# Performance work log

Measured on AMD Instinct MI355X. Metric: run time of the kernel, lower is better.

The kernel has to match this reference:

```python
import jax, jax.numpy as jnp
import numpy as np

B, C, H, W = 2, 192, 128, 128
NUM_HEADS = 6
AMP = 1
NUM_OFFSETS = 9


def bilinear_sample(img, grid):
    # img: (C, H, W); grid: (Hn, Wn, 2) in [-1,1], align_corners=True, zeros padding
    Hh, Ww = img.shape[1], img.shape[2]
    x = (grid[..., 0] + 1.0) * 0.5 * (Ww - 1)
    y = (grid[..., 1] + 1.0) * 0.5 * (Hh - 1)
    x0 = jnp.floor(x)
    y0 = jnp.floor(y)
    x1 = x0 + 1.0
    y1 = y0 + 1.0
    wx1 = x - x0
    wy1 = y - y0

    def gather(yi, xi):
        valid = ((xi >= 0) & (xi <= Ww - 1) & (yi >= 0) & (yi <= Hh - 1)).astype(img.dtype)
        xc = jnp.clip(xi, 0, Ww - 1).astype(jnp.int32)
        yc = jnp.clip(yi, 0, Hh - 1).astype(jnp.int32)
        return img[:, yc, xc] * valid  # (C, Hn, Wn)

    return (gather(y0, x0) * ((1 - wy1) * (1 - wx1))
            + gather(y0, x1) * ((1 - wy1) * wx1)
            + gather(y1, x0) * (wy1 * (1 - wx1))
            + gather(y1, x1) * (wy1 * wx1))


def setup_inputs() -> dict:
    key = jax.random.key(0)
    ks = jax.random.split(key, 8)
    s = 0.02
    Ch = C // NUM_HEADS
    return {
        "x_q": jax.random.normal(ks[0], (B, C, H, W), jnp.float32),
        "x_kv": jax.random.normal(ks[1], (B, C, H, W), jnp.float32),
        "w_q": jax.random.normal(ks[2], (C, C), jnp.float32) * s,
        "w_kv": jax.random.normal(ks[3], (2 * C, C), jnp.float32) * s,
        "w_off1": jax.random.normal(ks[4], (C, 2 * C, 3, 3), jnp.float32) * s,
        "b_off1": jnp.zeros((C,), jnp.float32),
        "w_off2": jax.random.normal(ks[5], (2 * NUM_OFFSETS, C), jnp.float32) * s,
        "b_off2": jnp.zeros((2 * NUM_OFFSETS,), jnp.float32),
        "w_proj": jax.random.normal(ks[6], (C, C), jnp.float32) * s,
        "b_proj": jnp.zeros((C,), jnp.float32),
    }


def reference(x_q, x_kv, w_q, w_kv, w_off1, b_off1, w_off2, b_off2, w_proj, b_proj):
    Ch = C // NUM_HEADS
    scale = Ch ** (-0.5)

    # 1x1 conv projections as channel matmuls
    q = jnp.einsum('oc,bchw->bohw', w_q, x_q) * scale
    kv = jnp.einsum('oc,bchw->bohw', w_kv, x_kv)
    k, v = kv[:, :C], kv[:, C:]  # kv.reshape(B,2,Ch,nh,H,W) -> first C channels are k

    # offset predictor: 3x3 conv -> relu -> 1x1 conv
    off_in = jnp.concatenate([x_q, x_kv], axis=1)
    h1 = jax.lax.conv_general_dilated(off_in, w_off1, (1, 1), 'SAME',
                                      dimension_numbers=('NCHW', 'OIHW', 'NCHW'))
    h1 = jax.nn.relu(h1 + b_off1[None, :, None, None])
    off = jnp.einsum('oc,bchw->bohw', w_off2, h1) + b_off2[None, :, None, None]
    off = off.reshape(B, NUM_OFFSETS, 2, H, W).transpose(0, 1, 3, 4, 2)  # (B,9,H,W,2)
    gx = off[..., 0] / (W - 1) * 2.0 - 1.0
    gy = off[..., 1] / (H - 1) * 2.0 - 1.0
    grid = jnp.stack([gx, gy], axis=-1)  # (B,9,H,W,2)

    # deformable gather: sample full-channel k/v at each of 9 per-pixel offset grids
    sample = jax.vmap(jax.vmap(bilinear_sample, in_axes=(None, 0)), in_axes=(0, 0))
    k_s = sample(k, grid).reshape(B, NUM_OFFSETS, Ch, NUM_HEADS, H, W)
    v_s = sample(v, grid).reshape(B, NUM_OFFSETS, Ch, NUM_HEADS, H, W)

    q = q.reshape(B, Ch, NUM_HEADS, H, W)

    pad = [(0, 0), (0, 0), (0, 0), (0, 0), (AMP, AMP), (AMP, AMP)]
    k_p = jnp.pad(k_s, pad)
    v_p = jnp.pad(v_s, pad)

    win = 2 * AMP + 1
    logits = []
    for i in range(win):
        for j in range(win):
            idx = i * win + j
            kp = k_p[:, idx, :, :, i:i + H, j:j + W]  # (B,Ch,nh,H,W)
            logits.append(jnp.einsum('bchxy,bchxy->bhxy', q, kp))
    attn = jax.nn.softmax(jnp.stack(logits, axis=1), axis=1)  # (B,9,nh,H,W)

    out = jnp.zeros((B, Ch, NUM_HEADS, H, W), x_q.dtype)
    for i in range(win):
        for j in range(win):
            idx = i * win + j
            vp = v_p[:, idx, :, :, i:i + H, j:j + W]
            out = out + attn[:, idx, None] * vp

    out = out.reshape(B, C, H, W)  # channel layout = (Ch, nh), matching torch reshape
    return jnp.einsum('oc,bchw->bohw', w_proj, out) + b_proj[None, :, None, None]
```

## Files before the change

kernel.cpp:

```cpp
#include <hip/hip_runtime.h>
#include <math.h>

#define HW 16384
#define NB 2
#define NC 192

typedef __attribute__((ext_vector_type(8))) short bh8;
typedef __attribute__((ext_vector_type(4))) float f32x4;

__device__ inline ushort f2bf(float f) {
  union { float f; unsigned int u; } x; x.f = f;
  unsigned int r = x.u + 0x7fffu + ((x.u >> 16) & 1u);
  return (ushort)(r >> 16);
}
__device__ inline float bf2f(ushort u) {
  union { unsigned int i; float f; } x; x.i = ((unsigned int)u) << 16;
  return x.f;
}
__device__ inline void gl16(const ushort* g, char* l) {
  __builtin_amdgcn_global_load_lds(
      (const __attribute__((address_space(1))) unsigned int*)g,
      (__attribute__((address_space(3))) unsigned int*)l, 16, 0, 0);
}

__global__ void k_wpack(const float* __restrict__ w1, ushort* __restrict__ wpack) {
  int i = blockIdx.x * 256 + threadIdx.x;
  int s = i / 6144;
  int rem = i - s * 6144;
  int o = rem >> 5, kk = rem & 31;
  int dy = s / 36, t2 = s - dy * 36;
  int icc = t2 / 3, dxi = t2 - icc * 3;
  int ic = icc * 32 + kk;
  wpack[i] = f2bf(w1[(size_t)o * 3456 + (size_t)ic * 9 + dy * 3 + dxi]);
}

__global__ void k_wgpack(const float* __restrict__ wq, const float* __restrict__ wkv,
                         const float* __restrict__ wp, float scale,
                         ushort* __restrict__ wg) {
  int i = blockIdx.x * 256 + threadIdx.x;
  int r = i / NC, c = i - r * NC;
  float v;
  if (r < 192) {
    int orow = (r & 31) * 6 + (r >> 5);
    v = wq[(size_t)orow * NC + c] * scale;
  } else if (r < 576) {
    int rp = r - 192;
    int t = rp >= 192 ? 1 : 0;
    int cc = rp - t * 192;
    int orow = t * 192 + (cc & 31) * 6 + (cc >> 5);
    v = wkv[(size_t)orow * NC + c];
  } else {
    int rp = r - 576;
    v = wp[(size_t)rp * NC + ((c & 31) * 6 + (c >> 5))];
  }
  wg[i] = f2bf(v);
}

__global__ void k_zero(uint4* __restrict__ p) {
  p[(size_t)blockIdx.x * 256 + threadIdx.x] = make_uint4(0u, 0u, 0u, 0u);
}

__global__ __launch_bounds__(256) void k_xpack(const float* __restrict__ xq,
                                               const float* __restrict__ xkv,
                                               ushort* __restrict__ xpp) {
  __shared__ float t[NC][65];
  const int tid = threadIdx.x;
  const size_t r0 = (size_t)blockIdx.x * 64;
  const int b = (int)(r0 >> 14);
  const int px0 = (int)(r0 & 16383);
  const int y = px0 >> 7, x0 = px0 & 127;
  const float* src = (blockIdx.y == 0 ? xq : xkv) + (size_t)b * NC * HW + px0;
#pragma unroll
  for (int it = 0; it < 12; ++it) {
    int i = it * 256 + tid;
    int c = i >> 4, q4 = i & 15;
    float4 v = *(const float4*)(src + (size_t)c * HW + q4 * 4);
    t[c][q4 * 4 + 0] = v.x; t[c][q4 * 4 + 1] = v.y;
    t[c][q4 * 4 + 2] = v.z; t[c][q4 * 4 + 3] = v.w;
  }
  __syncthreads();
  ushort* dst = xpp + ((size_t)(b * 130 + y + 1) * 132 + x0 + 1) * 384 +
                blockIdx.y * 192;
#pragma unroll
  for (int it = 0; it < 6; ++it) {
    int i = it * 256 + tid;
    int px = i / 24, ch = i - px * 24;
    ushort4 u0, u1;
    u0.x = f2bf(t[ch * 8 + 0][px]); u0.y = f2bf(t[ch * 8 + 1][px]);
    u0.z = f2bf(t[ch * 8 + 2][px]); u0.w = f2bf(t[ch * 8 + 3][px]);
    u1.x = f2bf(t[ch * 8 + 4][px]); u1.y = f2bf(t[ch * 8 + 5][px]);
    u1.z = f2bf(t[ch * 8 + 6][px]); u1.w = f2bf(t[ch * 8 + 7][px]);
    *(ushort4*)&dst[(size_t)px * 384 + ch * 8] = u0;
    *(ushort4*)&dst[(size_t)px * 384 + ch * 8 + 4] = u1;
  }
}

__device__ inline void stage64(ushort* lds, const ushort* src, int rowStride,
                               int tid) {
#pragma unroll
  for (int it = 0; it < 6; ++it) {
    int i = it * 256 + tid;
    int row = i / 24, c = i - row * 24;
    int pos = (c & 24) | ((c & 7) ^ (row & 7));
    uint4 v = *(const uint4*)(src + (size_t)row * rowStride + c * 8);
    *(uint4*)&lds[row * NC + pos * 8] = v;
  }
}
__device__ inline bh8 frag64(const ushort* lds, int row, int c) {
  int pos = (c & 24) | ((c & 7) ^ (row & 7));
  return *(const bh8*)&lds[row * NC + pos * 8];
}

__global__ __launch_bounds__(256) void k_gemm_mfma(
    const ushort* __restrict__ xpp, int cOff, const ushort* __restrict__ wg,
    ushort* __restrict__ outA, ushort* __restrict__ outB) {
  __shared__ __attribute__((aligned(16))) ushort xs[64 * NC];
  __shared__ __attribute__((aligned(16))) ushort ws2[64 * NC];
  const int tid = threadIdx.x;
  const size_t p0 = (size_t)blockIdx.x * 64;
  const int bb = (int)(p0 >> 14);
  const int yy = (int)((p0 >> 7) & 127);
  const int xx0 = (int)(p0 & 127);
  const int o0 = blockIdx.y * 64;
  const ushort* src = xpp + ((size_t)(bb * 130 + yy + 1) * 132 + xx0 + 1) * 384 + cOff;
  stage64(xs, src, 384, tid);
  stage64(ws2, wg + (size_t)o0 * NC, NC, tid);
  __syncthreads();
  const int lid = tid & 15, g = (tid >> 4) & 3, wv = tid >> 6;
  const int wo = (wv & 1) * 32, wp = (wv >> 1) * 32;
  f32x4 acc[2][2];
#pragma unroll
  for (int m = 0; m < 2; ++m)
#pragma unroll
    for (int n = 0; n < 2; ++n) acc[m][n] = (f32x4){0.f, 0.f, 0.f, 0.f};
#pragma unroll
  for (int k = 0; k < 6; ++k) {
    bh8 a0 = frag64(ws2, wo + lid, k * 4 + g);
    bh8 a1 = frag64(ws2, wo + 16 + lid, k * 4 + g);
    bh8 b0 = frag64(xs, wp + lid, k * 4 + g);
    bh8 b1 = frag64(xs, wp + 16 + lid, k * 4 + g);
    acc[0][0] = __builtin_amdgcn_mfma_f32_16x16x32_bf16(a0, b0, acc[0][0], 0, 0, 0);
    acc[0][1] = __builtin_amdgcn_mfma_f32_16x16x32_bf16(a0, b1, acc[0][1], 0, 0, 0);
    acc[1][0] = __builtin_amdgcn_mfma_f32_16x16x32_bf16(a1, b0, acc[1][0], 0, 0, 0);
    acc[1][1] = __builtin_amdgcn_mfma_f32_16x16x32_bf16(a1, b1, acc[1][1], 0, 0, 0);
  }
  const int t = o0 >= 192 ? 1 : 0;
  ushort* dst = t ? outB : outA;
  const int od = o0 - t * 192;
#pragma unroll
  for (int m = 0; m < 2; ++m)
#pragma unroll
    for (int n = 0; n < 2; ++n) {
      int orow = od + wo + m * 16 + g * 4;
      size_t px = p0 + wp + n * 16 + lid;
      ushort4 u;
      u.x = f2bf(acc[m][n][0]); u.y = f2bf(acc[m][n][1]);
      u.z = f2bf(acc[m][n][2]); u.w = f2bf(acc[m][n][3]);
      *(ushort4*)&dst[px * NC + orow] = u;
    }
}

__global__ __launch_bounds__(256) void k_proj_mfma(
    const ushort* __restrict__ pre, const ushort* __restrict__ wg,
    const float* __restrict__ bp, float* __restrict__ out) {
  __shared__ __attribute__((aligned(16))) ushort xs[64 * NC];
  __shared__ __attribute__((aligned(16))) ushort ws2[64 * NC];
  const int tid = threadIdx.x;
  const size_t p0 = (size_t)blockIdx.x * 64;
  const int o0 = blockIdx.y * 64;
  stage64(xs, pre + p0 * NC, NC, tid);
  stage64(ws2, wg + (size_t)o0 * NC, NC, tid);
  __syncthreads();
  const int lid = tid & 15, g = (tid >> 4) & 3, wv = tid >> 6;
  const int wo = (wv & 1) * 32, wp = (wv >> 1) * 32;
  f32x4 acc[2][2];
#pragma unroll
  for (int m = 0; m < 2; ++m)
#pragma unroll
    for (int n = 0; n < 2; ++n) acc[m][n] = (f32x4){0.f, 0.f, 0.f, 0.f};
#pragma unroll
  for (int k = 0; k < 6; ++k) {
    bh8 a0 = frag64(ws2, wo + lid, k * 4 + g);
    bh8 a1 = frag64(ws2, wo + 16 + lid, k * 4 + g);
    bh8 b0 = frag64(xs, wp + lid, k * 4 + g);
    bh8 b1 = frag64(xs, wp + 16 + lid, k * 4 + g);
    acc[0][0] = __builtin_amdgcn_mfma_f32_16x16x32_bf16(a0, b0, acc[0][0], 0, 0, 0);
    acc[0][1] = __builtin_amdgcn_mfma_f32_16x16x32_bf16(a0, b1, acc[0][1], 0, 0, 0);
    acc[1][0] = __builtin_amdgcn_mfma_f32_16x16x32_bf16(a1, b0, acc[1][0], 0, 0, 0);
    acc[1][1] = __builtin_amdgcn_mfma_f32_16x16x32_bf16(a1, b1, acc[1][1], 0, 0, 0);
  }
#pragma unroll
  for (int m = 0; m < 2; ++m)
#pragma unroll
    for (int n = 0; n < 2; ++n) {
      int oc = o0 + wo + m * 16 + g * 4;
      size_t pxf = p0 + wp + n * 16 + lid;
      int b = (int)(pxf >> 14);
      int px = (int)(pxf & 16383);
#pragma unroll
      for (int j = 0; j < 4; ++j)
        out[((size_t)b * NC + oc + j) * HW + px] = acc[m][n][j] + bp[oc + j];
    }
}

#define CP0 0
#define CP1 8448
#define CW0 16896
#define CW1 35328
__global__ __launch_bounds__(256, 3) void k_conv_mfma(
    const ushort* __restrict__ xpp, const ushort* __restrict__ wpack,
    const float* __restrict__ b1, ushort* __restrict__ h1) {
  __shared__ __attribute__((aligned(16))) char smem[53760];
  const int tid = threadIdx.x;
  const int bi = blockIdx.x;
  const int b = bi >> 8;
  const int y = (bi >> 1) & 127;
  const int oh = bi & 1;
  const int lid = tid & 15;
  const int g = (tid >> 4) & 3;
  const int wv = tid >> 6;
  const int lane = tid & 63;
  const int og = wv & 1;
  const int pg = wv >> 1;
  f32x4 acc[3][4];
#pragma unroll
  for (int m = 0; m < 3; ++m)
#pragma unroll
    for (int n = 0; n < 4; ++n) acc[m][n] = (f32x4){0.f, 0.f, 0.f, 0.f};

  auto stageP = [&](int icc, int dy, int buf) {
    const size_t rowbase = (size_t)(b * 130 + y + dy) * 132 * 384 + icc * 32;
    char* dst0 = smem + (buf ? CP1 : CP0);
    for (int grp = wv; grp < 9; grp += 4) {
      int i = grp * 64 + lane;
      if (i < 528) {
        int slot = i >> 2, ch = i & 3;
        gl16(xpp + rowbase + (size_t)slot * 384 + ((ch ^ ((slot >> 1) & 3)) << 3),
             dst0 + grp * 1024);
      }
    }
  };
  auto stageW = [&](int icc, int dy, int buf) {
    const ushort* wsrc = wpack + (size_t)((dy * 12 + icc) * 3) * 6144 + oh * 96 * 32;
    char* dst0 = smem + (buf ? CW1 : CW0);
    for (int grp = wv; grp < 18; grp += 4) {
      int i = grp * 64 + lane;
      int dxi = i / 384;
      int rem = i - dxi * 384;
      int o = rem >> 2, q = rem & 3;
      gl16(wsrc + (size_t)dxi * 6144 + o * 32 + ((q ^ ((o >> 1) & 3)) << 3),
           dst0 + grp * 1024);
    }
  };

  stageP(0, 0, 0);
  stageW(0, 0, 0);
  __syncthreads();
  int cur = 0;
  for (int s = 0; s < 36; ++s) {
    if (s < 35) {
      const int ns = s + 1;
      const int nicc = ns / 3, ndy = ns - nicc * 3;
      stageP(nicc, ndy, cur ^ 1);
      stageW(nicc, ndy, cur ^ 1);
    }
    const char* Pb = smem + (cur ? CP1 : CP0);
    const char* Wb = smem + (cur ? CW1 : CW0);
#pragma unroll
    for (int dxi = 0; dxi < 3; ++dxi) {
      bh8 af[3];
#pragma unroll
      for (int m = 0; m < 3; ++m) {
        int o = og * 48 + m * 16 + lid;
        af[m] = *(const bh8*)(Wb + ((dxi * 96 + o) << 6) +
                              ((g ^ ((o >> 1) & 3)) << 4));
      }
#pragma unroll
      for (int n = 0; n < 4; ++n) {
        int slot = pg * 64 + n * 16 + lid + dxi;
        bh8 bf = *(const bh8*)(Pb + (slot << 6) + ((g ^ ((slot >> 1) & 3)) << 4));
#pragma unroll
        for (int m = 0; m < 3; ++m)
          acc[m][n] = __builtin_amdgcn_mfma_f32_16x16x32_bf16(
              af[m], bf, acc[m][n], 0, 0, 0);
      }
    }
    __syncthreads();
    cur ^= 1;
  }

  const size_t pxbase = (size_t)(b << 14) + y * 128 + pg * 64;
#pragma unroll
  for (int m = 0; m < 3; ++m) {
    const int ob = oh * 96 + og * 48 + m * 16 + g * 4;
    float4 bv = *(const float4*)(b1 + ob);
#pragma unroll
    for (int n = 0; n < 4; ++n) {
      size_t px = pxbase + n * 16 + lid;
      h1[(size_t)(ob + 0) * (NB * HW) + px] = f2bf(fmaxf(acc[m][n][0] + bv.x, 0.f));
      h1[(size_t)(ob + 1) * (NB * HW) + px] = f2bf(fmaxf(acc[m][n][1] + bv.y, 0.f));
      h1[(size_t)(ob + 2) * (NB * HW) + px] = f2bf(fmaxf(acc[m][n][2] + bv.z, 0.f));
      h1[(size_t)(ob + 3) * (NB * HW) + px] = f2bf(fmaxf(acc[m][n][3] + bv.w, 0.f));
    }
  }
}

__global__ __launch_bounds__(256) void k_offhead(
    const ushort* __restrict__ h1, const float* __restrict__ w2,
    const float* __restrict__ b2, float* __restrict__ off) {
  __shared__ float w2l[18 * NC];
  const int tid = threadIdx.x;
  for (int i = tid; i < 18 * NC; i += 256) w2l[i] = w2[i];
  __syncthreads();
  const int px = tid & 127;
  const int jh = tid >> 7;
  const size_t p = (size_t)blockIdx.x * 128 + px;
  float acc[9];
#pragma unroll
  for (int jj = 0; jj < 9; ++jj) acc[jj] = b2[jh * 9 + jj];
  for (int c = 0; c < NC; ++c) {
    float v = bf2f(h1[(size_t)c * (NB * HW) + p]);
#pragma unroll
    for (int jj = 0; jj < 9; ++jj) acc[jj] += w2l[(jh * 9 + jj) * NC + c] * v;
  }
#pragma unroll
  for (int jj = 0; jj < 9; ++jj) off[p * 18 + jh * 9 + jj] = acc[jj];
}

__global__ __launch_bounds__(256) void k_attn(
    const ushort* __restrict__ q, const ushort* __restrict__ k,
    const ushort* __restrict__ v, const float* __restrict__ off,
    ushort* __restrict__ pre) {
  __shared__ float slog[4][6][9];
  __shared__ float sattn[4][6][9];
  const int wv = threadIdx.x >> 6;
  const int lane = threadIdx.x & 63;
  const size_t p = (size_t)blockIdx.x * 4 + wv;
  const int b = (int)(p >> 14);
  const int pp = (int)(p & 16383);
  const int y = pp >> 7, x = pp & 127;
  const ushort* qrow = q + p * NC;
  float qv0 = bf2f(qrow[lane]), qv1 = bf2f(qrow[lane + 64]), qv2 = bf2f(qrow[lane + 128]);
  float vsr[9][3];
#pragma unroll
  for (int idx = 0; idx < 9; ++idx) {
    const int di = idx / 3 - 1, dj = idx % 3 - 1;
    const int yy = y + di, xx = x + dj;
    const bool inb = (yy >= 0) && (yy < 128) && (xx >= 0) && (xx < 128);
    float ks0 = 0.f, ks1 = 0.f, ks2 = 0.f;
    float v0 = 0.f, v1 = 0.f, v2 = 0.f;
    if (inb) {
      const size_t sp = (size_t)b * HW + yy * 128 + xx;
      const float sx = off[sp * 18 + idx * 2 + 0];
      const float sy = off[sp * 18 + idx * 2 + 1];
      const float fx0 = floorf(sx), fy0 = floorf(sy);
      const float wx = sx - fx0, wy = sy - fy0;
#pragma unroll
      for (int cyx = 0; cyx < 4; ++cyx) {
        const int cy = cyx >> 1, cx = cyx & 1;
        const float xi = fx0 + cx, yi = fy0 + cy;
        const float wgt = (cx ? wx : 1.f - wx) * (cy ? wy : 1.f - wy);
        const bool okc = (xi >= 0.f) && (xi <= 127.f) && (yi >= 0.f) && (yi <= 127.f);
        if (okc) {
          const int xc = (int)xi, yc = (int)yi;
          const size_t cb = ((size_t)b * HW + yc * 128 + xc) * NC + lane;
          ks0 += wgt * bf2f(k[cb]);       v0 += wgt * bf2f(v[cb]);
          ks1 += wgt * bf2f(k[cb + 64]);  v1 += wgt * bf2f(v[cb + 64]);
          ks2 += wgt * bf2f(k[cb + 128]); v2 += wgt * bf2f(v[cb + 128]);
        }
      }
    }
    vsr[idx][0] = v0; vsr[idx][1] = v1; vsr[idx][2] = v2;
    float p0 = qv0 * ks0, p1 = qv1 * ks1, p2 = qv2 * ks2;
#pragma unroll
    for (int m = 16; m >= 1; m >>= 1) {
      p0 += __shfl_xor(p0, m);
      p1 += __shfl_xor(p1, m);
      p2 += __shfl_xor(p2, m);
    }
    if ((lane & 31) == 0) {
      const int hb = lane >> 5;
      slog[wv][hb + 0][idx] = p0;
      slog[wv][hb + 2][idx] = p1;
      slog[wv][hb + 4][idx] = p2;
    }
  }
  __syncthreads();
  if (lane < 6) {
    float mx = -1e30f;
#pragma unroll
    for (int i = 0; i < 9; ++i) mx = fmaxf(mx, slog[wv][lane][i]);
    float e[9];
    float s = 0.f;
#pragma unroll
    for (int i = 0; i < 9; ++i) { e[i] = expf(slog[wv][lane][i] - mx); s += e[i]; }
    const float inv = 1.f / s;
#pragma unroll
    for (int i = 0; i < 9; ++i) sattn[wv][lane][i] = e[i] * inv;
  }
  __syncthreads();
  float o0 = 0.f, o1 = 0.f, o2 = 0.f;
  const int hb = lane >> 5;
#pragma unroll
  for (int idx = 0; idx < 9; ++idx) {
    o0 += sattn[wv][hb + 0][idx] * vsr[idx][0];
    o1 += sattn[wv][hb + 2][idx] * vsr[idx][1];
    o2 += sattn[wv][hb + 4][idx] * vsr[idx][2];
  }
  ushort* prow = pre + p * NC;
  prow[lane] = f2bf(o0);
  prow[lane + 64] = f2bf(o1);
  prow[lane + 128] = f2bf(o2);
}

extern "C" void kernel_launch(void* const* d_in, const int* in_sizes, int n_in,
                              void* d_out, int out_size, void* d_ws, size_t ws_size,
                              hipStream_t stream) {
  const float* x_q    = (const float*)d_in[0];
  const float* x_kv   = (const float*)d_in[1];
  const float* w_q    = (const float*)d_in[2];
  const float* w_kv   = (const float*)d_in[3];
  const float* w_off1 = (const float*)d_in[4];
  const float* b_off1 = (const float*)d_in[5];
  const float* w_off2 = (const float*)d_in[6];
  const float* b_off2 = (const float*)d_in[7];
  const float* w_proj = (const float*)d_in[8];
  const float* b_proj = (const float*)d_in[9];
  float* out = (float*)d_out;

  char* W = (char*)d_ws;
  const size_t SB = (size_t)NB * HW * NC * 2;
  ushort* qb   = (ushort*)W;
  ushort* kb   = (ushort*)(W + SB);
  ushort* vb   = (ushort*)(W + 2 * SB);
  ushort* preb = (ushort*)(W + 3 * SB);
  ushort* h1b  = preb;
  ushort* wg   = (ushort*)(W + 4 * SB);
  ushort* xpp  = (ushort*)(W + 4 * SB + 294912);
  float*  offb = (float*)xpp;
  ushort* wpk  = (ushort*)d_out;

  const float scale = 0.17677669529663687f;
  dim3 blk(256);
  k_wpack<<<dim3(2592), blk, 0, stream>>>(w_off1, wpk);
  k_wgpack<<<dim3(576), blk, 0, stream>>>(w_q, w_kv, w_proj, scale, wg);
  k_zero<<<dim3(6435), blk, 0, stream>>>((uint4*)xpp);
  k_xpack<<<dim3(512, 2), blk, 0, stream>>>(x_q, x_kv, xpp);
  k_gemm_mfma<<<dim3(512, 3), blk, 0, stream>>>(xpp, 0, wg, qb, qb);
  k_gemm_mfma<<<dim3(512, 6), blk, 0, stream>>>(xpp, 192, wg + 192 * NC, kb, vb);
  k_conv_mfma<<<dim3(512), blk, 0, stream>>>(xpp, wpk, b_off1, h1b);
  k_offhead<<<dim3(NB * 128), blk, 0, stream>>>(h1b, w_off2, b_off2, offb);
  k_attn<<<dim3(8192), blk, 0, stream>>>(qb, kb, vb, offb, preb);
  k_proj_mfma<<<dim3(512, 3), blk, 0, stream>>>(preb, wg + 576 * NC, b_proj, out);
}
```

Baseline: 202.8 us.

## Vectorize deformable attention gathers and keep the softmax in registers

Each pixel's work is remapped so 48 lanes each own 4 contiguous bf16 channels. The q, k and v corner gathers become 8-byte vector loads, and the per-head dot products are reduced with three shuffles inside each 8-lane group. The shared-memory logits and attention buffers and both __syncthreads are removed, and the corner gathers use clamped indices with mask weights instead of branches. The intent is fewer, wider memory transactions and less synchronization. In exchange, 16 lanes per wave sit idle and the code uses fast exp and reciprocal intrinsics, which may change precision slightly.

```diff
diff --git a/kernel.cpp b/kernel.cpp
--- a/kernel.cpp
+++ b/kernel.cpp
@@ -16,6 +16,9 @@
 __device__ inline float bf2f(ushort u) {
   union { unsigned int i; float f; } x; x.i = ((unsigned int)u) << 16;
   return x.f;
+}
+__device__ inline float asf(unsigned int u) {
+  union { unsigned int i; float f; } x; x.i = u; return x.f;
 }
 __device__ inline void gl16(const ushort* g, char* l) {
   __builtin_amdgcn_global_load_lds(
@@ -331,86 +334,96 @@
     const ushort* __restrict__ q, const ushort* __restrict__ k,
     const ushort* __restrict__ v, const float* __restrict__ off,
     ushort* __restrict__ pre) {
-  __shared__ float slog[4][6][9];
-  __shared__ float sattn[4][6][9];
   const int wv = threadIdx.x >> 6;
   const int lane = threadIdx.x & 63;
+  if (lane >= 48) return;
   const size_t p = (size_t)blockIdx.x * 4 + wv;
   const int b = (int)(p >> 14);
   const int pp = (int)(p & 16383);
   const int y = pp >> 7, x = pp & 127;
-  const ushort* qrow = q + p * NC;
-  float qv0 = bf2f(qrow[lane]), qv1 = bf2f(qrow[lane + 64]), qv2 = bf2f(qrow[lane + 128]);
-  float vsr[9][3];
+
+  uint2 qu = *(const uint2*)(q + p * NC + 4 * lane);
+  const float q0 = asf(qu.x << 16), q1 = asf(qu.x & 0xffff0000u);
+  const float q2 = asf(qu.y << 16), q3 = asf(qu.y & 0xffff0000u);
+  const size_t cbase = (size_t)b * HW * NC + 4 * lane;
+  const size_t obase = (size_t)b * HW;
+
+  float pl[9];
+  float vsr[9][4];
 #pragma unroll
   for (int idx = 0; idx < 9; ++idx) {
-    const int di = idx / 3 - 1, dj = idx % 3 - 1;
-    const int yy = y + di, xx = x + dj;
+    const int yy = y + idx / 3 - 1, xx = x + idx % 3 - 1;
     const bool inb = (yy >= 0) && (yy < 128) && (xx >= 0) && (xx < 128);
-    float ks0 = 0.f, ks1 = 0.f, ks2 = 0.f;
-    float v0 = 0.f, v1 = 0.f, v2 = 0.f;
+    float sx = 0.f, sy = 0.f;
     if (inb) {
-      const size_t sp = (size_t)b * HW + yy * 128 + xx;
-      const float sx = off[sp * 18 + idx * 2 + 0];
-      const float sy = off[sp * 18 + idx * 2 + 1];
-      const float fx0 = floorf(sx), fy0 = floorf(sy);
-      const float wx = sx - fx0, wy = sy - fy0;
-#pragma unroll
-      for (int cyx = 0; cyx < 4; ++cyx) {
-        const int cy = cyx >> 1, cx = cyx & 1;
-        const float xi = fx0 + cx, yi = fy0 + cy;
-        const float wgt = (cx ? wx : 1.f - wx) * (cy ? wy : 1.f - wy);
-        const bool okc = (xi >= 0.f) && (xi <= 127.f) && (yi >= 0.f) && (yi <= 127.f);
-        if (okc) {
-          const int xc = (int)xi, yc = (int)yi;
-          const size_t cb = ((size_t)b * HW + yc * 128 + xc) * NC + lane;
-          ks0 += wgt * bf2f(k[cb]);       v0 += wgt * bf2f(v[cb]);
-          ks1 += wgt * bf2f(k[cb + 64]);  v1 += wgt * bf2f(v[cb + 64]);
-          ks2 += wgt * bf2f(k[cb + 128]); v2 += wgt * bf2f(v[cb + 128]);
-        }
-      }
-    }
-    vsr[idx][0] = v0; vsr[idx][1] = v1; vsr[idx][2] = v2;
-    float p0 = qv0 * ks0, p1 = qv1 * ks1, p2 = qv2 * ks2;
-#pragma unroll
-    for (int m = 16; m >= 1; m >>= 1) {
-      p0 += __shfl_xor(p0, m);
-      p1 += __shfl_xor(p1, m);
-      p2 += __shfl_xor(p2, m);
-    }
-    if ((lane & 31) == 0) {
-      const int hb = lane >> 5;
-      slog[wv][hb + 0][idx] = p0;
-      slog[wv][hb + 2][idx] = p1;
-      slog[wv][hb + 4][idx] = p2;
-    }
-  }
-  __syncthreads();
-  if (lane < 6) {
-    float mx = -1e30f;
-#pragma unroll
-    for (int i = 0; i < 9; ++i) mx = fmaxf(mx, slog[wv][lane][i]);
-    float e[9];
-    float s = 0.f;
-#pragma unroll
-    for (int i = 0; i < 9; ++i) { e[i] = expf(slog[wv][lane][i] - mx); s += e[i]; }
-    const float inv = 1.f / s;
-#pragma unroll
-    for (int i = 0; i < 9; ++i) sattn[wv][lane][i] = e[i] * inv;
-  }
-  __syncthreads();
-  float o0 = 0.f, o1 = 0.f, o2 = 0.f;
-  const int hb = lane >> 5;
-#pragma unroll
-  for (int idx = 0; idx < 9; ++idx) {
-    o0 += sattn[wv][hb + 0][idx] * vsr[idx][0];
-    o1 += sattn[wv][hb + 2][idx] * vsr[idx][1];
-    o2 += sattn[wv][hb + 4][idx] * vsr[idx][2];
-  }
-  ushort* prow = pre + p * NC;
-  prow[lane] = f2bf(o0);
-  prow[lane + 64] = f2bf(o1);
-  prow[lane + 128] = f2bf(o2);
+      const size_t sp = obase + yy * 128 + xx;
+      sx = off[sp * 18 + idx * 2 + 0];
+      sy = off[sp * 18 + idx * 2 + 1];
+    }
+    const float fx0 = floorf(sx), fy0 = floorf(sy);
+    const float wx1 = sx - fx0, wy1 = sy - fy0;
+    const float wx0 = 1.f - wx1, wy0 = 1.f - wy1;
+    const float inbf = inb ? 1.f : 0.f;
+    const float mx0 = (fx0 >= 0.f && fx0 <= 127.f) ? inbf : 0.f;
+    const float mx1 = (fx0 >= -1.f && fx0 <= 126.f) ? inbf : 0.f;
+    const float my0 = (fy0 >= 0.f && fy0 <= 127.f) ? 1.f : 0.f;
+    const float my1 = (fy0 >= -1.f && fy0 <= 126.f) ? 1.f : 0.f;
+    const int ix0 = (int)fminf(fmaxf(fx0, 0.f), 127.f);
+    const int iy0 = (int)fminf(fmaxf(fy0, 0.f), 127.f);
+    const int ix1 = (int)fminf(fmaxf(fx0 + 1.f, 0.f), 127.f);
+    const int iy1 = (int)fminf(fmaxf(fy0 + 1.f, 0.f), 127.f);
+    const float w00 = wy0 * wx0 * my0 * mx0, w01 = wy0 * wx1 * my0 * mx1;
+    const float w10 = wy1 * wx0 * my1 * mx0, w11 = wy1 * wx1 * my1 * mx1;
+    const size_t e00 = cbase + (size_t)(iy0 * 128 + ix0) * NC;
+    const size_t e01 = cbase + (size_t)(iy0 * 128 + ix1) * NC;
+    const size_t e10 = cbase + (size_t)(iy1 * 128 + ix0) * NC;
+    const size_t e11 = cbase + (size_t)(iy1 * 128 + ix1) * NC;
+    float ks0 = 0.f, ks1 = 0.f, ks2 = 0.f, ks3 = 0.f;
+    float vs0 = 0.f, vs1 = 0.f, vs2 = 0.f, vs3 = 0.f;
+#define CORNER(W, E)                                            \
+  {                                                             \
+    uint2 kk = *(const uint2*)(k + (E));                        \
+    uint2 vvv = *(const uint2*)(v + (E));                       \
+    ks0 = fmaf((W), asf(kk.x << 16), ks0);                      \
+    ks1 = fmaf((W), asf(kk.x & 0xffff0000u), ks1);              \
+    ks2 = fmaf((W), asf(kk.y << 16), ks2);                      \
+    ks3 = fmaf((W), asf(kk.y & 0xffff0000u), ks3);              \
+    vs0 = fmaf((W), asf(vvv.x << 16), vs0);                     \
+    vs1 = fmaf((W), asf(vvv.x & 0xffff0000u), vs1);             \
+    vs2 = fmaf((W), asf(vvv.y << 16), vs2);                     \
+    vs3 = fmaf((W), asf(vvv.y & 0xffff0000u), vs3);             \
+  }
+    CORNER(w00, e00)
+    CORNER(w01, e01)
+    CORNER(w10, e10)
+    CORNER(w11, e11)
+#undef CORNER
+    float pd = q0 * ks0 + q1 * ks1 + q2 * ks2 + q3 * ks3;
+    pd += __shfl_xor(pd, 1);
+    pd += __shfl_xor(pd, 2);
+    pd += __shfl_xor(pd, 4);
+    pl[idx] = pd;
+    vsr[idx][0] = vs0; vsr[idx][1] = vs1; vsr[idx][2] = vs2; vsr[idx][3] = vs3;
+  }
+  float mx = pl[0];
+#pragma unroll
+  for (int i = 1; i < 9; ++i) mx = fmaxf(mx, pl[i]);
+  float s = 0.f;
+#pragma unroll
+  for (int i = 0; i < 9; ++i) { pl[i] = __expf(pl[i] - mx); s += pl[i]; }
+  const float inv = __builtin_amdgcn_rcpf(s);
+  float o0 = 0.f, o1 = 0.f, o2 = 0.f, o3 = 0.f;
+#pragma unroll
+  for (int i = 0; i < 9; ++i) {
+    const float a = pl[i] * inv;
+    o0 = fmaf(a, vsr[i][0], o0);
+    o1 = fmaf(a, vsr[i][1], o1);
+    o2 = fmaf(a, vsr[i][2], o2);
+    o3 = fmaf(a, vsr[i][3], o3);
+  }
+  ushort4 r;
+  r.x = f2bf(o0); r.y = f2bf(o1); r.z = f2bf(o2); r.w = f2bf(o3);
+  *(ushort4*)(pre + p * NC + 4 * lane) = r;
 }
 
 extern "C" void kernel_launch(void* const* d_in, const int* in_sizes, int n_in,
```

New measurement: 225.1 us. 1.11x slower.
